# Kernel tuning notes

Measured on AMD Instinct MI355X. Metric: run time of the kernel, lower is better.

Reference implementation:

```python
import jax, jax.numpy as jnp
import numpy as np

N_HEAD = 16


def setup_inputs() -> dict:
    key = jax.random.key(0)
    ks = jax.random.split(key, 6)
    B, T, C = 2, 2048, 1024
    hs = C // N_HEAD  # 64
    block_minus_1 = 2048  # block_size - 1
    x = jax.random.normal(ks[0], (B, T, C), dtype=jnp.float32)
    W1 = jax.random.normal(ks[1], (C, C), dtype=jnp.float32) * (1.0 / np.sqrt(C))
    b1 = jnp.zeros((C,), dtype=jnp.float32)
    # original init: uniform(-1e-3, 1e-3)
    w2 = jax.random.uniform(ks[2], (hs, block_minus_1), dtype=jnp.float32, minval=-1e-3, maxval=1e-3)
    b2 = jnp.zeros((block_minus_1,), dtype=jnp.float32)
    Wv = jax.random.normal(ks[3], (C, C), dtype=jnp.float32) * (1.0 / np.sqrt(C))
    bv = jnp.zeros((C,), dtype=jnp.float32)
    Wp = jax.random.normal(ks[4], (C, C), dtype=jnp.float32) * (1.0 / np.sqrt(C))
    bp = jnp.zeros((C,), dtype=jnp.float32)
    return {"x": x, "W1": W1, "b1": b1, "w2": w2, "b2": b2,
            "Wv": Wv, "bv": bv, "Wp": Wp, "bp": bp}


def reference(x, W1, b1, w2, b2, Wv, bv, Wp, bp):
    B, T, C = x.shape
    hs = C // N_HEAD
    r = jax.nn.relu(x @ W1.T + b1).reshape(B, T, N_HEAD, hs).transpose(0, 2, 1, 3)
    # synthesizer scores: (B, nh, T, T) = relu_out @ w2[:, :T] + b2[:T]
    att = jnp.einsum('bhtd,dj->bhtj', r, w2[:, :T]) + b2[:T]
    causal = jnp.tril(jnp.ones((T, T), dtype=bool))
    att = jnp.where(causal[None, None], att, jnp.float32(-1e10))
    att = jax.nn.softmax(att, axis=-1)  # attn_drop = 0 (eval)
    v = (x @ Wv.T + bv).reshape(B, T, N_HEAD, hs).transpose(0, 2, 1, 3)
    y = jnp.einsum('bhtj,bhjd->bhtd', att, v)
    y = y.transpose(0, 2, 1, 3).reshape(B, T, C)
    return y @ Wp.T + bp  # resid_drop = 0 (eval)
```

## Files before the change

### kernel.cpp

```cpp
#include <hip/hip_runtime.h>

typedef __bf16 bf16x8 __attribute__((ext_vector_type(8)));
typedef float f32x4 __attribute__((ext_vector_type(4)));

__device__ __forceinline__ unsigned short f2bf(float f) {
  union { float f; unsigned u; } v; v.f = f;
  unsigned u = v.u;
  return (unsigned short)((u + 0x7fffu + ((u >> 16) & 1u)) >> 16);
}
__device__ __forceinline__ unsigned short f2bf_fast(float f) {
  union { float f; unsigned u; } v; v.f = f;
  return (unsigned short)((v.u + 0x8000u) >> 16);
}
__device__ __forceinline__ void gload_lds16(const void* g, void* l) {
  __builtin_amdgcn_global_load_lds(
      (const __attribute__((address_space(1))) unsigned int*)g,
      (__attribute__((address_space(3))) unsigned int*)l, 16, 0, 0);
}
__device__ __forceinline__ void cvt4(const float* __restrict__ s,
                                     unsigned short* __restrict__ d, int u) {
  f32x4 v = ((const f32x4*)s)[u];
  union { unsigned short s[4]; unsigned long long u; } o;
  o.s[0] = f2bf(v[0]); o.s[1] = f2bf(v[1]); o.s[2] = f2bf(v[2]); o.s[3] = f2bf(v[3]);
  ((unsigned long long*)d)[u] = o.u;
}


__global__ void prep(const float* __restrict__ x, const float* __restrict__ W1,
                     const float* __restrict__ Wv, const float* __restrict__ Wp,
                     const float* __restrict__ w2, const float* __restrict__ b2,
                     unsigned short* __restrict__ xb, unsigned short* __restrict__ W1b,
                     unsigned short* __restrict__ Wvb, unsigned short* __restrict__ Wpb,
                     unsigned short* __restrict__ w2t, unsigned short* __restrict__ ebj) {
  int u = blockIdx.x * 256 + threadIdx.x;
  if (u < 1048576) { cvt4(x, xb, u); return; }
  u -= 1048576;
  if (u < 262144) { cvt4(W1, W1b, u); return; }
  u -= 262144;
  if (u < 262144) { cvt4(Wv, Wvb, u); return; }
  u -= 262144;
  if (u < 262144) { cvt4(Wp, Wpb, u); return; }
  u -= 262144;
  if (u < 32768) {
    int j = u >> 4, d4 = (u & 15) * 4;
    union { unsigned short s[4]; unsigned long long x; } o;
#pragma unroll
    for (int i = 0; i < 4; ++i) o.s[i] = f2bf(w2[(d4 + i) * 2048 + j]);
    ((unsigned long long*)w2t)[u] = o.x;
    return;
  }
  u -= 32768;
  union { unsigned short s[4]; unsigned long long x; } o;
#pragma unroll
  for (int i = 0; i < 4; ++i) o.s[i] = f2bf(__expf(b2[u * 4 + i]));
  ((unsigned long long*)ebj)[u] = o.x;
}

__global__ __launch_bounds__(256) void gemm_rv(
    const unsigned short* __restrict__ xb, const unsigned short* __restrict__ W1b,
    const unsigned short* __restrict__ Wvb, const float* __restrict__ b1,
    const float* __restrict__ bv, const float* __restrict__ b2,
    unsigned short* __restrict__ rb, unsigned short* __restrict__ vtb) {
  __shared__ unsigned short As[128 * 64];
  __shared__ unsigned short Bs[128 * 64];
  int id = blockIdx.x;
  const unsigned short *A, *Bt;
  const float* bias;
  unsigned short* C;
  int N, tileM, tileN, epi;
  if (id < 256) {
    A = xb; Bt = W1b; bias = b1; C = rb; N = 1024; epi = 0;
    tileN = (id & 7) * 128; tileM = (id >> 3) * 128;
  } else {
    id -= 256;
    A = Wvb; Bt = xb; bias = bv; C = vtb; N = 4096; epi = 1;
    tileN = (id & 31) * 128; tileM = (id >> 5) * 128;
  }
  const int tid = threadIdx.x;
  const int wv = tid >> 6, ln = tid & 63;
  const int quad = ln >> 4, lq = ln & 15;
  const int wr = wv >> 1, wc = wv & 1;
  const int rowL = ln >> 3;
  const int kc = (((ln & 7) ^ rowL) & 7) * 8;
  const int sx = lq & 7;
  const int ko0 = (quad ^ sx) * 8, ko1 = ((4 + quad) ^ sx) * 8;

  f32x4 acc[4][4];
  const f32x4 zf = {0.f, 0.f, 0.f, 0.f};
#pragma unroll
  for (int i = 0; i < 4; ++i)
#pragma unroll
    for (int j = 0; j < 4; ++j) acc[i][j] = zf;

  for (int k0 = 0; k0 < 1024; k0 += 64) {
    __syncthreads();
#pragma unroll
    for (int l = 0; l < 4; ++l) {
      int row = l * 32 + wv * 8 + rowL;
      gload_lds16(A + (tileM + row) * 1024 + k0 + kc, &As[l * 2048 + wv * 512]);
      gload_lds16(Bt + (tileN + row) * 1024 + k0 + kc, &Bs[l * 2048 + wv * 512]);
    }
    __syncthreads();
#pragma unroll
    for (int kk = 0; kk < 2; ++kk) {
      const int ko = kk ? ko1 : ko0;
      bf16x8 af[4], bfr[4];
#pragma unroll
      for (int mi = 0; mi < 4; ++mi)
        af[mi] = *(const bf16x8*)&As[(wr * 64 + mi * 16 + lq) * 64 + ko];
#pragma unroll
      for (int ni = 0; ni < 4; ++ni)
        bfr[ni] = *(const bf16x8*)&Bs[(wc * 64 + ni * 16 + lq) * 64 + ko];
#pragma unroll
      for (int mi = 0; mi < 4; ++mi)
#pragma unroll
        for (int ni = 0; ni < 4; ++ni)
          acc[mi][ni] = __builtin_amdgcn_mfma_f32_16x16x32_bf16(af[mi], bfr[ni], acc[mi][ni], 0, 0, 0);
    }
  }
#pragma unroll
  for (int ni = 0; ni < 4; ++ni) {
    int col = tileN + wc * 64 + ni * 16 + lq;
    float eb = (epi == 1) ? __expf(b2[col & 2047]) : 0.0f;
#pragma unroll
    for (int mi = 0; mi < 4; ++mi) {
#pragma unroll
      for (int rg = 0; rg < 4; ++rg) {
        int row = tileM + wr * 64 + mi * 16 + quad * 4 + rg;
        float v = acc[mi][ni][rg];
        if (epi == 0) {
          v += bias[col];
          v = v > 0.f ? v : 0.f;
        } else {
          v = (v + bias[row]) * eb;
        }
        C[row * N + col] = f2bf(v);
      }
    }
  }
}

__global__ __launch_bounds__(256) void gemm_p(
    const unsigned short* __restrict__ A, const unsigned short* __restrict__ Bt,
    const float* __restrict__ bias, float* __restrict__ C) {
  __shared__ unsigned short As[128 * 64];
  __shared__ unsigned short Bs[64 * 64];
  const int tid = threadIdx.x;
  const int wv = tid >> 6, ln = tid & 63;
  const int quad = ln >> 4, lq = ln & 15;
  const int tileM = blockIdx.y * 128, tileN = blockIdx.x * 64;
  const int rowL = ln >> 3;
  const int kc = (((ln & 7) ^ rowL) & 7) * 8;
  const int sx = lq & 7;
  const int ko0 = (quad ^ sx) * 8, ko1 = ((4 + quad) ^ sx) * 8;

  f32x4 acc[2][4];
  const f32x4 zf = {0.f, 0.f, 0.f, 0.f};
#pragma unroll
  for (int i = 0; i < 2; ++i)
#pragma unroll
    for (int j = 0; j < 4; ++j) acc[i][j] = zf;

  for (int k0 = 0; k0 < 1024; k0 += 64) {
    __syncthreads();
#pragma unroll
    for (int l = 0; l < 4; ++l) {
      int row = l * 32 + wv * 8 + rowL;
      gload_lds16(A + (tileM + row) * 1024 + k0 + kc, &As[l * 2048 + wv * 512]);
    }
#pragma unroll
    for (int l = 0; l < 2; ++l) {
      int row = l * 32 + wv * 8 + rowL;
      gload_lds16(Bt + (tileN + row) * 1024 + k0 + kc, &Bs[l * 2048 + wv * 512]);
    }
    __syncthreads();
#pragma unroll
    for (int kk = 0; kk < 2; ++kk) {
      const int ko = kk ? ko1 : ko0;
      bf16x8 af[2], bfr[4];
#pragma unroll
      for (int mi = 0; mi < 2; ++mi)
        af[mi] = *(const bf16x8*)&As[(wv * 32 + mi * 16 + lq) * 64 + ko];
#pragma unroll
      for (int ni = 0; ni < 4; ++ni)
        bfr[ni] = *(const bf16x8*)&Bs[(ni * 16 + lq) * 64 + ko];
#pragma unroll
      for (int mi = 0; mi < 2; ++mi)
#pragma unroll
        for (int ni = 0; ni < 4; ++ni)
          acc[mi][ni] = __builtin_amdgcn_mfma_f32_16x16x32_bf16(af[mi], bfr[ni], acc[mi][ni], 0, 0, 0);
    }
  }
#pragma unroll
  for (int mi = 0; mi < 2; ++mi)
#pragma unroll
    for (int ni = 0; ni < 4; ++ni) {
      int col = tileN + ni * 16 + lq;
#pragma unroll
      for (int rg = 0; rg < 4; ++rg) {
        int row = tileM + wv * 32 + mi * 16 + quad * 4 + rg;
        C[row * 1024 + col] = acc[mi][ni][rg] + bias[col];
      }
    }
}

__global__ __launch_bounds__(256, 4) void attn(
    const unsigned short* __restrict__ r, const unsigned short* __restrict__ w2t,
    const unsigned short* __restrict__ vt, const unsigned short* __restrict__ ebj,
    unsigned short* __restrict__ y) {
  __shared__ unsigned short W2s[2][64 * 64];
  __shared__ unsigned short Vs[2][64 * 64];
  __shared__ unsigned short Ps[4][16 * 64];

  const int tid = threadIdx.x;
  const int wv = tid >> 6, ln = tid & 63;
  const int quad = ln >> 4, lq = ln & 15;
  const int bh = blockIdx.y, b = bh >> 4, h = bh & 15;
  const int tt = (31 - blockIdx.x + blockIdx.y) & 31;
  const int rowL = ln >> 3;
  const int kc = (((ln & 7) ^ rowL) & 7) * 8;
  const int sx = lq & 7;
  const int ko0 = (quad ^ sx) * 8, ko1 = ((4 + quad) ^ sx) * 8;
  const int t0 = tt * 64;

  bf16x8 ra0, ra1;
  {
    const unsigned short* base = r + (b * 2048 + t0 + wv * 16 + lq) * 1024 + h * 64 + quad * 8;
    ra0 = *(const bf16x8*)(base);
    ra1 = *(const bf16x8*)(base + 32);
  }

  f32x4 accY[4];
  f32x4 accL;
  const f32x4 zf = {0.f, 0.f, 0.f, 0.f};
#pragma unroll
  for (int nd = 0; nd < 4; ++nd) accY[nd] = zf;
  accL = zf;

  auto stage = [&](int jt, int bi) {
    int j0 = jt * 64;
#pragma unroll
    for (int l = 0; l < 2; ++l) {
      int row = l * 32 + wv * 8 + rowL;
      gload_lds16(w2t + (j0 + row) * 64 + kc, &W2s[bi][l * 2048 + wv * 512]);
      gload_lds16(vt + (h * 64 + row) * 4096 + b * 2048 + j0 + kc,
                  &Vs[bi][l * 2048 + wv * 512]);
    }
  };

  stage(0, 0);
  for (int jt = 0; jt <= tt; ++jt) {
    const int cb = jt & 1;
    __syncthreads();
    if (jt < tt) stage(jt + 1, cb ^ 1);
    const int j0 = jt * 64;

    bf16x8 eb0 = *(const bf16x8*)&ebj[j0 + quad * 8];
    bf16x8 eb1 = *(const bf16x8*)&ebj[j0 + 32 + quad * 8];
    bf16x8 w2f0[4], w2f1[4];
#pragma unroll
    for (int ni = 0; ni < 4; ++ni) {
      w2f0[ni] = *(const bf16x8*)&W2s[cb][(ni * 16 + lq) * 64 + ko0];
      w2f1[ni] = *(const bf16x8*)&W2s[cb][(ni * 16 + lq) * 64 + ko1];
    }

    f32x4 sv[4] = {zf, zf, zf, zf};
#pragma unroll
    for (int ni = 0; ni < 4; ++ni) {
      sv[ni] = __builtin_amdgcn_mfma_f32_16x16x32_bf16(ra0, w2f0[ni], sv[ni], 0, 0, 0);
      sv[ni] = __builtin_amdgcn_mfma_f32_16x16x32_bf16(ra1, w2f1[ni], sv[ni], 0, 0, 0);
    }

    const bool diag = (jt == tt);
#pragma unroll
    for (int ni = 0; ni < 4; ++ni) {
      int j = j0 + ni * 16 + lq;
#pragma unroll
      for (int rg = 0; rg < 4; ++rg) {
        float p = __expf(sv[ni][rg]);
        if (diag) {
          int t = t0 + wv * 16 + quad * 4 + rg;
          p = (j <= t) ? p : 0.f;
        }
        Ps[wv][(quad * 4 + rg) * 64 +
               (((ni * 2 + (lq >> 3)) ^ ((quad * 4 + rg) & 7)) * 8) + (lq & 7)] = f2bf_fast(p);
      }
    }

#pragma unroll
    for (int kk = 0; kk < 2; ++kk) {
      const int ko = kk ? ko1 : ko0;
      bf16x8 pa = *(const bf16x8*)&Ps[wv][lq * 64 + ko];
#pragma unroll
      for (int nd = 0; nd < 4; ++nd) {
        bf16x8 bb = *(const bf16x8*)&Vs[cb][(nd * 16 + lq) * 64 + ko];
        accY[nd] = __builtin_amdgcn_mfma_f32_16x16x32_bf16(pa, bb, accY[nd], 0, 0, 0);
      }
      accL = __builtin_amdgcn_mfma_f32_16x16x32_bf16(pa, kk ? eb1 : eb0, accL, 0, 0, 0);
    }
  }

  float inv[4];
#pragma unroll
  for (int rg = 0; rg < 4; ++rg) inv[rg] = __builtin_amdgcn_rcpf(accL[rg]);
#pragma unroll
  for (int nd = 0; nd < 4; ++nd)
#pragma unroll
    for (int rg = 0; rg < 4; ++rg) {
      int t = t0 + wv * 16 + quad * 4 + rg;
      y[(b * 2048 + t) * 1024 + h * 64 + nd * 16 + lq] = f2bf(accY[nd][rg] * inv[rg]);
    }
}

extern "C" void kernel_launch(void* const* d_in, const int* in_sizes, int n_in,
                              void* d_out, int out_size, void* d_ws, size_t ws_size,
                              hipStream_t stream) {
  const float* x  = (const float*)d_in[0];
  const float* W1 = (const float*)d_in[1];
  const float* b1 = (const float*)d_in[2];
  const float* w2 = (const float*)d_in[3];
  const float* b2 = (const float*)d_in[4];
  const float* Wv = (const float*)d_in[5];
  const float* bv = (const float*)d_in[6];
  const float* Wp = (const float*)d_in[7];
  const float* bp = (const float*)d_in[8];

  unsigned short* ws  = (unsigned short*)d_ws;
  unsigned short* xb   = ws;
  unsigned short* W1b  = ws + 4194304;
  unsigned short* Wvb  = ws + 5242880;
  unsigned short* Wpb  = ws + 6291456;
  unsigned short* w2t  = ws + 7340032;
  unsigned short* rb   = ws + 7471104;
  unsigned short* vt   = ws + 11665408;
  unsigned short* yb   = ws + 15859712;
  unsigned short* ebjb = ws + 20054016;

  prep<<<7298, 256, 0, stream>>>(x, W1, Wv, Wp, w2, b2, xb, W1b, Wvb, Wpb, w2t, ebjb);
  gemm_rv<<<512, 256, 0, stream>>>(xb, W1b, Wvb, b1, bv, b2, rb, vt);
  attn<<<dim3(32, 32), 256, 0, stream>>>(rb, w2t, vt, ebjb, yb);
  gemm_p<<<dim3(16, 32), 256, 0, stream>>>(yb, Wpb, bp, (float*)d_out);
}
```

Measured before the change: 192.5 us.

## Pair complementary causal tiles per block and read w2 directly from global

The attention kernel now uses 128-thread blocks of two waves, each wave handling 16 query rows. One wave takes tile p and the other takes tile 31-p, so every block does a balanced amount of causal work. V tiles are still staged through LDS and shared by both waves, while the W2 tile is now loaded per wave straight from global memory (relying on cache) instead of being staged in LDS. This targets load imbalance across the causal triangle and cuts LDS use, at the cost of more blocks, less V reuse per staged tile, and waves idling at barriers once their own range is finished.

```diff
diff --git a/kernel.cpp b/kernel.cpp
--- a/kernel.cpp
+++ b/kernel.cpp
@@ -204,28 +204,31 @@
     }
 }
 
-__global__ __launch_bounds__(256, 4) void attn(
+__global__ __launch_bounds__(128, 4) void attn(
     const unsigned short* __restrict__ r, const unsigned short* __restrict__ w2t,
     const unsigned short* __restrict__ vt, const unsigned short* __restrict__ ebj,
     unsigned short* __restrict__ y) {
-  __shared__ unsigned short W2s[2][64 * 64];
   __shared__ unsigned short Vs[2][64 * 64];
-  __shared__ unsigned short Ps[4][16 * 64];
+  __shared__ unsigned short Ps[2][16 * 64];
 
   const int tid = threadIdx.x;
   const int wv = tid >> 6, ln = tid & 63;
   const int quad = ln >> 4, lq = ln & 15;
+  const int pp = blockIdx.x & 15, s = blockIdx.x >> 4;
   const int bh = blockIdx.y, b = bh >> 4, h = bh & 15;
-  const int tt = (31 - blockIdx.x + blockIdx.y) & 31;
+  const int p = (pp + bh) & 15;
+  const int myTile = wv ? (31 - p) : p;
+  const int myJT = myTile;
+  const int jhi = 31 - p;
+  const int t0 = myTile * 64 + s * 16;
   const int rowL = ln >> 3;
   const int kc = (((ln & 7) ^ rowL) & 7) * 8;
   const int sx = lq & 7;
   const int ko0 = (quad ^ sx) * 8, ko1 = ((4 + quad) ^ sx) * 8;
-  const int t0 = tt * 64;
 
   bf16x8 ra0, ra1;
   {
-    const unsigned short* base = r + (b * 2048 + t0 + wv * 16 + lq) * 1024 + h * 64 + quad * 8;
+    const unsigned short* base = r + (b * 2048 + t0 + lq) * 1024 + h * 64 + quad * 8;
     ra0 = *(const bf16x8*)(base);
     ra1 = *(const bf16x8*)(base + 32);
   }
@@ -240,63 +243,63 @@
   auto stage = [&](int jt, int bi) {
     int j0 = jt * 64;
 #pragma unroll
-    for (int l = 0; l < 2; ++l) {
-      int row = l * 32 + wv * 8 + rowL;
-      gload_lds16(w2t + (j0 + row) * 64 + kc, &W2s[bi][l * 2048 + wv * 512]);
-      gload_lds16(vt + (h * 64 + row) * 4096 + b * 2048 + j0 + kc,
-                  &Vs[bi][l * 2048 + wv * 512]);
+    for (int l = 0; l < 4; ++l) {
+      gload_lds16(vt + (h * 64 + wv * 32 + l * 8 + rowL) * 4096 + b * 2048 + j0 + kc,
+                  &Vs[bi][(wv * 32 + l * 8) * 64]);
     }
   };
 
   stage(0, 0);
-  for (int jt = 0; jt <= tt; ++jt) {
+  for (int jt = 0; jt <= jhi; ++jt) {
     const int cb = jt & 1;
     __syncthreads();
-    if (jt < tt) stage(jt + 1, cb ^ 1);
-    const int j0 = jt * 64;
-
-    bf16x8 eb0 = *(const bf16x8*)&ebj[j0 + quad * 8];
-    bf16x8 eb1 = *(const bf16x8*)&ebj[j0 + 32 + quad * 8];
-    bf16x8 w2f0[4], w2f1[4];
-#pragma unroll
-    for (int ni = 0; ni < 4; ++ni) {
-      w2f0[ni] = *(const bf16x8*)&W2s[cb][(ni * 16 + lq) * 64 + ko0];
-      w2f1[ni] = *(const bf16x8*)&W2s[cb][(ni * 16 + lq) * 64 + ko1];
-    }
-
-    f32x4 sv[4] = {zf, zf, zf, zf};
-#pragma unroll
-    for (int ni = 0; ni < 4; ++ni) {
-      sv[ni] = __builtin_amdgcn_mfma_f32_16x16x32_bf16(ra0, w2f0[ni], sv[ni], 0, 0, 0);
-      sv[ni] = __builtin_amdgcn_mfma_f32_16x16x32_bf16(ra1, w2f1[ni], sv[ni], 0, 0, 0);
-    }
-
-    const bool diag = (jt == tt);
-#pragma unroll
-    for (int ni = 0; ni < 4; ++ni) {
-      int j = j0 + ni * 16 + lq;
-#pragma unroll
-      for (int rg = 0; rg < 4; ++rg) {
-        float p = __expf(sv[ni][rg]);
-        if (diag) {
-          int t = t0 + wv * 16 + quad * 4 + rg;
-          p = (j <= t) ? p : 0.f;
+    if (jt < jhi) stage(jt + 1, cb ^ 1);
+    if (jt <= myJT) {
+      const int j0 = jt * 64;
+      bf16x8 eb0 = *(const bf16x8*)&ebj[j0 + quad * 8];
+      bf16x8 eb1 = *(const bf16x8*)&ebj[j0 + 32 + quad * 8];
+      bf16x8 w2f0[4], w2f1[4];
+#pragma unroll
+      for (int ni = 0; ni < 4; ++ni) {
+        const unsigned short* wb = &w2t[(j0 + ni * 16 + lq) * 64 + quad * 8];
+        w2f0[ni] = *(const bf16x8*)(wb);
+        w2f1[ni] = *(const bf16x8*)(wb + 32);
+      }
+
+      f32x4 sv[4] = {zf, zf, zf, zf};
+#pragma unroll
+      for (int ni = 0; ni < 4; ++ni) {
+        sv[ni] = __builtin_amdgcn_mfma_f32_16x16x32_bf16(ra0, w2f0[ni], sv[ni], 0, 0, 0);
+        sv[ni] = __builtin_amdgcn_mfma_f32_16x16x32_bf16(ra1, w2f1[ni], sv[ni], 0, 0, 0);
+      }
+
+      const bool diag = (jt == myJT);
+#pragma unroll
+      for (int ni = 0; ni < 4; ++ni) {
+        int j = j0 + ni * 16 + lq;
+#pragma unroll
+        for (int rg = 0; rg < 4; ++rg) {
+          float pex = __expf(sv[ni][rg]);
+          if (diag) {
+            int t = t0 + quad * 4 + rg;
+            pex = (j <= t) ? pex : 0.f;
+          }
+          Ps[wv][(quad * 4 + rg) * 64 +
+                 (((ni * 2 + (lq >> 3)) ^ ((quad * 4 + rg) & 7)) * 8) + (lq & 7)] = f2bf_fast(pex);
         }
-        Ps[wv][(quad * 4 + rg) * 64 +
-               (((ni * 2 + (lq >> 3)) ^ ((quad * 4 + rg) & 7)) * 8) + (lq & 7)] = f2bf_fast(p);
-      }
-    }
-
-#pragma unroll
-    for (int kk = 0; kk < 2; ++kk) {
-      const int ko = kk ? ko1 : ko0;
-      bf16x8 pa = *(const bf16x8*)&Ps[wv][lq * 64 + ko];
-#pragma unroll
-      for (int nd = 0; nd < 4; ++nd) {
-        bf16x8 bb = *(const bf16x8*)&Vs[cb][(nd * 16 + lq) * 64 + ko];
-        accY[nd] = __builtin_amdgcn_mfma_f32_16x16x32_bf16(pa, bb, accY[nd], 0, 0, 0);
-      }
-      accL = __builtin_amdgcn_mfma_f32_16x16x32_bf16(pa, kk ? eb1 : eb0, accL, 0, 0, 0);
+      }
+
+#pragma unroll
+      for (int kk = 0; kk < 2; ++kk) {
+        const int ko = kk ? ko1 : ko0;
+        bf16x8 pa = *(const bf16x8*)&Ps[wv][lq * 64 + ko];
+#pragma unroll
+        for (int nd = 0; nd < 4; ++nd) {
+          bf16x8 bb = *(const bf16x8*)&Vs[cb][(nd * 16 + lq) * 64 + ko];
+          accY[nd] = __builtin_amdgcn_mfma_f32_16x16x32_bf16(pa, bb, accY[nd], 0, 0, 0);
+        }
+        accL = __builtin_amdgcn_mfma_f32_16x16x32_bf16(pa, kk ? eb1 : eb0, accL, 0, 0, 0);
+      }
     }
   }
 
@@ -307,7 +310,7 @@
   for (int nd = 0; nd < 4; ++nd)
 #pragma unroll
     for (int rg = 0; rg < 4; ++rg) {
-      int t = t0 + wv * 16 + quad * 4 + rg;
+      int t = t0 + quad * 4 + rg;
       y[(b * 2048 + t) * 1024 + h * 64 + nd * 16 + lq] = f2bf(accY[nd][rg] * inv[rg]);
     }
 }
@@ -338,6 +341,6 @@
 
   prep<<<7298, 256, 0, stream>>>(x, W1, Wv, Wp, w2, b2, xb, W1b, Wvb, Wpb, w2t, ebjb);
   gemm_rv<<<512, 256, 0, stream>>>(xb, W1b, Wvb, b1, bv, b2, rb, vt);
-  attn<<<dim3(32, 32), 256, 0, stream>>>(rb, w2t, vt, ebjb, yb);
+  attn<<<dim3(64, 32), 128, 0, stream>>>(rb, w2t, vt, ebjb, yb);
   gemm_p<<<dim3(16, 32), 256, 0, stream>>>(yb, Wpb, bp, (float*)d_out);
 }
```

After: 220.1 us. 1.14x slower.

## Shrink gemm_rv tiles to 128x64 and restage attn V in 128-column chunks

Applied to the files above, without the earlier changes.

gemm_rv moves from 128x128 to 128x64 output tiles, so the grid doubles to 1024 blocks and each wave covers a 32x64 slab. The aim is better occupancy and load balance on the many-CU device, paid for with more A-tile reloads. In attn, the W2 tile is no longer staged in LDS and is read straight from global/L2 per wave. V is now staged 128 keys at a time with a new XOR swizzle, and two 64-key tiles are processed per barrier to halve syncs. Ps store offsets are precomputed into registers, which raises register pressure.

```diff
diff --git a/kernel.cpp b/kernel.cpp
--- a/kernel.cpp
+++ b/kernel.cpp
@@ -62,33 +62,32 @@
     const float* __restrict__ bv, const float* __restrict__ b2,
     unsigned short* __restrict__ rb, unsigned short* __restrict__ vtb) {
   __shared__ unsigned short As[128 * 64];
-  __shared__ unsigned short Bs[128 * 64];
+  __shared__ unsigned short Bs[64 * 64];
   int id = blockIdx.x;
   const unsigned short *A, *Bt;
   const float* bias;
   unsigned short* C;
   int N, tileM, tileN, epi;
-  if (id < 256) {
+  if (id < 512) {
     A = xb; Bt = W1b; bias = b1; C = rb; N = 1024; epi = 0;
-    tileN = (id & 7) * 128; tileM = (id >> 3) * 128;
+    tileN = (id & 15) * 64; tileM = (id >> 4) * 128;
   } else {
-    id -= 256;
+    id -= 512;
     A = Wvb; Bt = xb; bias = bv; C = vtb; N = 4096; epi = 1;
-    tileN = (id & 31) * 128; tileM = (id >> 5) * 128;
+    tileN = (id & 63) * 64; tileM = (id >> 6) * 128;
   }
   const int tid = threadIdx.x;
   const int wv = tid >> 6, ln = tid & 63;
   const int quad = ln >> 4, lq = ln & 15;
-  const int wr = wv >> 1, wc = wv & 1;
   const int rowL = ln >> 3;
   const int kc = (((ln & 7) ^ rowL) & 7) * 8;
   const int sx = lq & 7;
   const int ko0 = (quad ^ sx) * 8, ko1 = ((4 + quad) ^ sx) * 8;
 
-  f32x4 acc[4][4];
+  f32x4 acc[2][4];
   const f32x4 zf = {0.f, 0.f, 0.f, 0.f};
 #pragma unroll
-  for (int i = 0; i < 4; ++i)
+  for (int i = 0; i < 2; ++i)
 #pragma unroll
     for (int j = 0; j < 4; ++j) acc[i][j] = zf;
 
@@ -98,21 +97,25 @@
     for (int l = 0; l < 4; ++l) {
       int row = l * 32 + wv * 8 + rowL;
       gload_lds16(A + (tileM + row) * 1024 + k0 + kc, &As[l * 2048 + wv * 512]);
+    }
+#pragma unroll
+    for (int l = 0; l < 2; ++l) {
+      int row = l * 32 + wv * 8 + rowL;
       gload_lds16(Bt + (tileN + row) * 1024 + k0 + kc, &Bs[l * 2048 + wv * 512]);
     }
     __syncthreads();
 #pragma unroll
     for (int kk = 0; kk < 2; ++kk) {
       const int ko = kk ? ko1 : ko0;
-      bf16x8 af[4], bfr[4];
-#pragma unroll
-      for (int mi = 0; mi < 4; ++mi)
-        af[mi] = *(const bf16x8*)&As[(wr * 64 + mi * 16 + lq) * 64 + ko];
+      bf16x8 af[2], bfr[4];
+#pragma unroll
+      for (int mi = 0; mi < 2; ++mi)
+        af[mi] = *(const bf16x8*)&As[(wv * 32 + mi * 16 + lq) * 64 + ko];
 #pragma unroll
       for (int ni = 0; ni < 4; ++ni)
-        bfr[ni] = *(const bf16x8*)&Bs[(wc * 64 + ni * 16 + lq) * 64 + ko];
-#pragma unroll
-      for (int mi = 0; mi < 4; ++mi)
+        bfr[ni] = *(const bf16x8*)&Bs[(ni * 16 + lq) * 64 + ko];
+#pragma unroll
+      for (int mi = 0; mi < 2; ++mi)
 #pragma unroll
         for (int ni = 0; ni < 4; ++ni)
           acc[mi][ni] = __builtin_amdgcn_mfma_f32_16x16x32_bf16(af[mi], bfr[ni], acc[mi][ni], 0, 0, 0);
@@ -120,13 +123,13 @@
   }
 #pragma unroll
   for (int ni = 0; ni < 4; ++ni) {
-    int col = tileN + wc * 64 + ni * 16 + lq;
+    int col = tileN + ni * 16 + lq;
     float eb = (epi == 1) ? __expf(b2[col & 2047]) : 0.0f;
 #pragma unroll
-    for (int mi = 0; mi < 4; ++mi) {
+    for (int mi = 0; mi < 2; ++mi) {
 #pragma unroll
       for (int rg = 0; rg < 4; ++rg) {
-        int row = tileM + wr * 64 + mi * 16 + quad * 4 + rg;
+        int row = tileM + wv * 32 + mi * 16 + quad * 4 + rg;
         float v = acc[mi][ni][rg];
         if (epi == 0) {
           v += bias[col];
@@ -208,8 +211,7 @@
     const unsigned short* __restrict__ r, const unsigned short* __restrict__ w2t,
     const unsigned short* __restrict__ vt, const unsigned short* __restrict__ ebj,
     unsigned short* __restrict__ y) {
-  __shared__ unsigned short W2s[2][64 * 64];
-  __shared__ unsigned short Vs[2][64 * 64];
+  __shared__ unsigned short Vs[2][64 * 128];
   __shared__ unsigned short Ps[4][16 * 64];
 
   const int tid = threadIdx.x;
@@ -217,8 +219,6 @@
   const int quad = ln >> 4, lq = ln & 15;
   const int bh = blockIdx.y, b = bh >> 4, h = bh & 15;
   const int tt = (31 - blockIdx.x + blockIdx.y) & 31;
-  const int rowL = ln >> 3;
-  const int kc = (((ln & 7) ^ rowL) & 7) * 8;
   const int sx = lq & 7;
   const int ko0 = (quad ^ sx) * 8, ko1 = ((4 + quad) ^ sx) * 8;
   const int t0 = tt * 64;
@@ -230,6 +230,14 @@
     ra1 = *(const bf16x8*)(base + 32);
   }
 
+  int psoff[4][4];
+#pragma unroll
+  for (int ni = 0; ni < 4; ++ni)
+#pragma unroll
+    for (int rg = 0; rg < 4; ++rg)
+      psoff[ni][rg] = (quad * 4 + rg) * 64 +
+                      (((ni * 2 + (lq >> 3)) ^ ((quad * 4 + rg) & 7)) * 8) + (lq & 7);
+
   f32x4 accY[4];
   f32x4 accL;
   const f32x4 zf = {0.f, 0.f, 0.f, 0.f};
@@ -237,67 +245,73 @@
   for (int nd = 0; nd < 4; ++nd) accY[nd] = zf;
   accL = zf;
 
-  auto stage = [&](int jt, int bi) {
-    int j0 = jt * 64;
-#pragma unroll
-    for (int l = 0; l < 2; ++l) {
-      int row = l * 32 + wv * 8 + rowL;
-      gload_lds16(w2t + (j0 + row) * 64 + kc, &W2s[bi][l * 2048 + wv * 512]);
-      gload_lds16(vt + (h * 64 + row) * 4096 + b * 2048 + j0 + kc,
-                  &Vs[bi][l * 2048 + wv * 512]);
+  auto stage = [&](int ji, int bi) {
+    int j0 = ji * 128;
+#pragma unroll
+    for (int l = 0; l < 4; ++l) {
+      int row = wv * 16 + l * 4 + (ln >> 4);
+      int sc = (ln & 15) ^ (row & 7);
+      gload_lds16(vt + (h * 64 + row) * 4096 + b * 2048 + j0 + sc * 8,
+                  &Vs[bi][(wv * 16 + l * 4) * 128]);
     }
   };
 
+  const int nIter = (tt >> 1) + 1;
   stage(0, 0);
-  for (int jt = 0; jt <= tt; ++jt) {
-    const int cb = jt & 1;
-    __syncthreads();
-    if (jt < tt) stage(jt + 1, cb ^ 1);
-    const int j0 = jt * 64;
-
-    bf16x8 eb0 = *(const bf16x8*)&ebj[j0 + quad * 8];
-    bf16x8 eb1 = *(const bf16x8*)&ebj[j0 + 32 + quad * 8];
-    bf16x8 w2f0[4], w2f1[4];
-#pragma unroll
-    for (int ni = 0; ni < 4; ++ni) {
-      w2f0[ni] = *(const bf16x8*)&W2s[cb][(ni * 16 + lq) * 64 + ko0];
-      w2f1[ni] = *(const bf16x8*)&W2s[cb][(ni * 16 + lq) * 64 + ko1];
-    }
-
-    f32x4 sv[4] = {zf, zf, zf, zf};
-#pragma unroll
-    for (int ni = 0; ni < 4; ++ni) {
-      sv[ni] = __builtin_amdgcn_mfma_f32_16x16x32_bf16(ra0, w2f0[ni], sv[ni], 0, 0, 0);
-      sv[ni] = __builtin_amdgcn_mfma_f32_16x16x32_bf16(ra1, w2f1[ni], sv[ni], 0, 0, 0);
-    }
-
-    const bool diag = (jt == tt);
-#pragma unroll
-    for (int ni = 0; ni < 4; ++ni) {
-      int j = j0 + ni * 16 + lq;
-#pragma unroll
-      for (int rg = 0; rg < 4; ++rg) {
-        float p = __expf(sv[ni][rg]);
-        if (diag) {
-          int t = t0 + wv * 16 + quad * 4 + rg;
-          p = (j <= t) ? p : 0.f;
+  for (int ji = 0; ji < nIter; ++ji) {
+    const int cb = ji & 1;
+    __syncthreads();
+    if (ji + 1 < nIter) stage(ji + 1, cb ^ 1);
+
+    auto tilebody = [&](int jt) {
+      const int j0t = jt * 64;
+      const int jh = jt & 1;
+      bf16x8 eb0 = *(const bf16x8*)&ebj[j0t + quad * 8];
+      bf16x8 eb1 = *(const bf16x8*)&ebj[j0t + 32 + quad * 8];
+      bf16x8 w2f0[4], w2f1[4];
+#pragma unroll
+      for (int ni = 0; ni < 4; ++ni) {
+        const unsigned short* wb = &w2t[(j0t + ni * 16 + lq) * 64 + quad * 8];
+        w2f0[ni] = *(const bf16x8*)(wb);
+        w2f1[ni] = *(const bf16x8*)(wb + 32);
+      }
+      f32x4 sv[4] = {zf, zf, zf, zf};
+#pragma unroll
+      for (int ni = 0; ni < 4; ++ni) {
+        sv[ni] = __builtin_amdgcn_mfma_f32_16x16x32_bf16(ra0, w2f0[ni], sv[ni], 0, 0, 0);
+        sv[ni] = __builtin_amdgcn_mfma_f32_16x16x32_bf16(ra1, w2f1[ni], sv[ni], 0, 0, 0);
+      }
+      const bool diag = (jt == tt);
+#pragma unroll
+      for (int ni = 0; ni < 4; ++ni) {
+        int j = j0t + ni * 16 + lq;
+#pragma unroll
+        for (int rg = 0; rg < 4; ++rg) {
+          float p = __expf(sv[ni][rg]);
+          if (diag) {
+            int t = t0 + wv * 16 + quad * 4 + rg;
+            p = (j <= t) ? p : 0.f;
+          }
+          Ps[wv][psoff[ni][rg]] = f2bf_fast(p);
         }
-        Ps[wv][(quad * 4 + rg) * 64 +
-               (((ni * 2 + (lq >> 3)) ^ ((quad * 4 + rg) & 7)) * 8) + (lq & 7)] = f2bf_fast(p);
-      }
-    }
-
-#pragma unroll
-    for (int kk = 0; kk < 2; ++kk) {
-      const int ko = kk ? ko1 : ko0;
-      bf16x8 pa = *(const bf16x8*)&Ps[wv][lq * 64 + ko];
-#pragma unroll
-      for (int nd = 0; nd < 4; ++nd) {
-        bf16x8 bb = *(const bf16x8*)&Vs[cb][(nd * 16 + lq) * 64 + ko];
-        accY[nd] = __builtin_amdgcn_mfma_f32_16x16x32_bf16(pa, bb, accY[nd], 0, 0, 0);
-      }
-      accL = __builtin_amdgcn_mfma_f32_16x16x32_bf16(pa, kk ? eb1 : eb0, accL, 0, 0, 0);
-    }
+      }
+#pragma unroll
+      for (int kk = 0; kk < 2; ++kk) {
+        const int ko = kk ? ko1 : ko0;
+        const int vko = ((jh * 8 + kk * 4 + quad) ^ sx) * 8;
+        bf16x8 pa = *(const bf16x8*)&Ps[wv][lq * 64 + ko];
+#pragma unroll
+        for (int nd = 0; nd < 4; ++nd) {
+          bf16x8 bb = *(const bf16x8*)&Vs[cb][(nd * 16 + lq) * 128 + vko];
+          accY[nd] = __builtin_amdgcn_mfma_f32_16x16x32_bf16(pa, bb, accY[nd], 0, 0, 0);
+        }
+        accL = __builtin_amdgcn_mfma_f32_16x16x32_bf16(pa, kk ? eb1 : eb0, accL, 0, 0, 0);
+      }
+    };
+
+    const int jt0 = ji * 2;
+    tilebody(jt0);
+    if (jt0 + 1 <= tt) tilebody(jt0 + 1);
   }
 
   float inv[4];
@@ -337,7 +351,7 @@
   unsigned short* ebjb = ws + 20054016;
 
   prep<<<7298, 256, 0, stream>>>(x, W1, Wv, Wp, w2, b2, xb, W1b, Wvb, Wpb, w2t, ebjb);
-  gemm_rv<<<512, 256, 0, stream>>>(xb, W1b, Wvb, b1, bv, b2, rb, vt);
+  gemm_rv<<<1024, 256, 0, stream>>>(xb, W1b, Wvb, b1, bv, b2, rb, vt);
   attn<<<dim3(32, 32), 256, 0, stream>>>(rb, w2t, vt, ebjb, yb);
   gemm_p<<<dim3(16, 32), 256, 0, stream>>>(yb, Wpb, bp, (float*)d_out);
 }
```

Result: slower. 229.3 us (+19.2%).
